# Kernel tuning notes

Measured on AMD Instinct MI355X. Metric: run time of the kernel, lower is better.

The kernel has to match this reference:

```python
import jax, jax.numpy as jnp
import numpy as np

N, T, IN, HID, ST, NL, OUT = 256, 2048, 6, 128, 64, 2, 6
LAY = IN + HID  # LMSCCell layer_size = input_size + hidden_size


def setup_inputs() -> dict:
    key = jax.random.key(0)
    ks = jax.random.split(key, 8)

    def w(k, shape, fan_in):
        return jax.random.normal(k, shape, jnp.float32) / np.sqrt(fan_in).astype(np.float32)

    return {
        "X": jax.random.normal(ks[0], (N, T, IN), jnp.float32),
        "H0": jax.random.normal(ks[1], (N, ST), jnp.float32),
        # NL gated layers (layer_size -> layer_size), stored stacked, weights as (in, out)
        "Wg1": w(ks[2], (NL, LAY, LAY), LAY), "bg1": jnp.zeros((NL, LAY), jnp.float32),
        "Wg2": w(ks[3], (NL, LAY, LAY), LAY), "bg2": jnp.zeros((NL, LAY), jnp.float32),
        # final pair: alpha (exp) and beta (tanh), layer_size -> hidden
        "Wa": w(ks[4], (LAY, HID), LAY), "ba": jnp.zeros((HID,), jnp.float32),
        "Wb": w(ks[5], (LAY, HID), LAY), "bb": jnp.zeros((HID,), jnp.float32),
        # hstate: Linear(state_size -> hidden) producing S0
        "Wh": w(ks[6], (ST, HID), ST), "bh": jnp.zeros((HID,), jnp.float32),
        # sstate2: Linear(hidden -> out_size)
        "Wo": w(ks[7], (HID, OUT), HID), "bo": jnp.zeros((OUT,), jnp.float32),
    }


def reference(X, H0, Wg1, bg1, Wg2, bg2, Wa, ba, Wb, bb, Wh, bh, Wo, bo):
    # hstate: initial hidden state for the LMSC recurrence
    S0 = H0 @ Wh + bh  # (N, HID)

    def step(H, x_t):
        # x_t: (N, IN); H: (N, HID)
        norm = jnp.linalg.norm(x_t, axis=1, keepdims=True)  # (N, 1)
        Lv = jnp.concatenate([x_t / norm, H], axis=1)       # (N, LAY)
        for i in range(NL):  # small fixed layer count, structurally distinct weights
            Lv = jnp.tanh(Lv @ Wg1[i] + bg1[i]) * jnp.tanh(Lv @ Wg2[i] + bg2[i])
        alpha = jnp.exp(Lv @ Wa + ba)   # (N, HID)
        beta = jnp.tanh(Lv @ Wb + bb)   # (N, HID)
        Hn = jnp.exp(-alpha * norm) * (H - beta) + beta
        return Hn, Hn

    _, Ys = jax.lax.scan(step, S0, jnp.swapaxes(X, 0, 1))  # (T, N, HID)
    Y = jnp.swapaxes(Ys, 0, 1)  # (N, T, HID)
    return Y @ Wo + bo          # (N, T, OUT)
```

## Files before the change

### kernel.cpp

```cpp
#include <hip/hip_runtime.h>

#define Nb   256
#define Tt   2048
#define INs  6
#define HID  128
#define STs  64
#define LAY  134
#define OUTs 6
#define NPAIR 67
#define NDW  68

typedef _Float16 h2 __attribute__((ext_vector_type(2)));
typedef __fp16  f16x2 __attribute__((ext_vector_type(2)));

__device__ __forceinline__ float exp2_fast(float x) {
#if __has_builtin(__builtin_amdgcn_exp2f)
    return __builtin_amdgcn_exp2f(x);
#else
    return exp2f(x);
#endif
}
__device__ __forceinline__ float rcp_fast(float x) {
#if __has_builtin(__builtin_amdgcn_rcpf)
    return __builtin_amdgcn_rcpf(x);
#else
    return 1.0f / x;
#endif
}
__device__ __forceinline__ float tanh_fast(float x) {
    float e = exp2_fast(x * 2.8853900817779268f);
    return 1.0f - 2.0f * rcp_fast(e + 1.0f);
}
__device__ __forceinline__ unsigned pack2(float a, float b) {
#if __has_builtin(__builtin_amdgcn_cvt_pkrtz)
    union { f16x2 h; unsigned u; } u;
    u.h = __builtin_amdgcn_cvt_pkrtz(a, b);
    return u.u;
#else
    union { h2 h; unsigned u; } u;
    u.h[0] = (_Float16)a; u.h[1] = (_Float16)b;
    return u.u;
#endif
}
__device__ __forceinline__ h2 as_h2(unsigned v) {
    union { unsigned u; h2 h; } u; u.u = v; return u.h;
}
__device__ __forceinline__ float dot2f(h2 a, h2 b, float c) {
#if __has_builtin(__builtin_amdgcn_fdot2)
    union { h2 h; f16x2 f; } ua, ub;
    ua.h = a; ub.h = b;
    return __builtin_amdgcn_fdot2(ua.f, ub.f, c, false);
#else
    return c + (float)a[0] * (float)b[0] + (float)a[1] * (float)b[1];
#endif
}

__device__ __forceinline__ float dotLv(const unsigned* buf, const h2* w, float bias) {
    const uint4* b4 = (const uint4*)buf;
    float a0 = 0.f, a1 = 0.f, a2 = 0.f, a3 = 0.f;
#pragma unroll
    for (int m = 0; m < 17; ++m) {
        uint4 v = b4[m];
        a0 = dot2f(as_h2(v.x), w[4*m+0], a0);
        a1 = dot2f(as_h2(v.y), w[4*m+1], a1);
        a2 = dot2f(as_h2(v.z), w[4*m+2], a2);
        a3 = dot2f(as_h2(v.w), w[4*m+3], a3);
    }
    return ((a0 + a1) + (a2 + a3)) + bias;
}

__device__ __forceinline__ void do_proj(const float* Hrow, const float* wo0, const float* wo1,
                                        const float* bo6, float* outp, int l) {
    float hA = Hrow[2*l], hB = Hrow[2*l+1];
    float r[6];
#pragma unroll
    for (int o = 0; o < 6; ++o) r[o] = hA * wo0[o] + hB * wo1[o];
#pragma unroll
    for (int o = 0; o < 6; ++o) {
#pragma unroll
        for (int k = 1; k < 64; k <<= 1) r[o] += __shfl_xor(r[o], k, 64);
    }
    if (l == 0) {
#pragma unroll
        for (int o = 0; o < 6; ++o) outp[o] = r[o] + bo6[o];
    }
}

__global__ __launch_bounds__(1024)
void lmsc_kernel(const float* __restrict__ X,  const float* __restrict__ H0,
                 const float* __restrict__ Wg1, const float* __restrict__ bg1,
                 const float* __restrict__ Wg2, const float* __restrict__ bg2,
                 const float* __restrict__ Wa,  const float* __restrict__ ba,
                 const float* __restrict__ Wb,  const float* __restrict__ bb,
                 const float* __restrict__ Wh,  const float* __restrict__ bh,
                 const float* __restrict__ Wo,  const float* __restrict__ bo,
                 float* __restrict__ out)
{
    __shared__ float Xls[Tt * INs];
    __shared__ alignas(16) unsigned LvX[NDW];
    __shared__ alignas(16) unsigned LvB[NDW];
    __shared__ float T1[LAY], T2[LAY];
    __shared__ float Hf[2][HID];
    __shared__ float Aal[HID], Bbe[HID];
    __shared__ float H0l[STs];
    __shared__ float nrm[2], rnr[2];

    const int tid = threadIdx.x;
    const int n   = blockIdx.x;

    {
        const float4* Xg  = (const float4*)(X + (size_t)n * (Tt * INs));
        float4*       Xl4 = (float4*)Xls;
        for (int i = tid; i < (Tt * INs) / 4; i += 1024) Xl4[i] = Xg[i];
    }
    if (tid < STs) H0l[tid] = H0[n * STs + tid];

    h2 wreg[NDW];
    float bias = 0.f;
    {
        const float* Wp = nullptr; int od = LAY, j = 0;
        if      (tid < 134) { Wp = Wg1;             j = tid;       bias = bg1[j]; }
        else if (tid < 268) { Wp = Wg2;             j = tid - 134; bias = bg2[j]; }
        else if (tid < 402) { Wp = Wg1 + LAY*LAY;   j = tid - 268; bias = bg1[LAY + j]; }
        else if (tid < 536) { Wp = Wg2 + LAY*LAY;   j = tid - 402; bias = bg2[LAY + j]; }
        else if (tid < 664) { Wp = Wa; od = HID;    j = tid - 536; bias = ba[j]; }
        else if (tid < 792) { Wp = Wb; od = HID;    j = tid - 664; bias = bb[j]; }
        if (Wp) {
            for (int m = 0; m < NPAIR; ++m) {
                float w0 = Wp[(2*m)     * od + j];
                float w1 = Wp[(2*m + 1) * od + j];
                h2 h; h[0] = (_Float16)w0; h[1] = (_Float16)w1;
                wreg[m] = h;
            }
            h2 z; z[0] = (_Float16)0.f; z[1] = (_Float16)0.f;
            wreg[NPAIR] = z;
        }
    }
    float wo0[6], wo1[6], bo6[6];
    if (tid >= 960) {
        int l = tid - 960;
#pragma unroll
        for (int o = 0; o < 6; ++o) {
            wo0[o] = Wo[(2*l)     * OUTs + o];
            wo1[o] = Wo[(2*l + 1) * OUTs + o];
            bo6[o] = bo[o];
        }
    }
    __syncthreads();

    if (tid >= 536 && tid < 664) {
        int j = tid - 536;
        float s = bh[j];
        for (int k = 0; k < STs; ++k) s += H0l[k] * Wh[k * HID + j];
        Hf[0][j] = s;
        ((_Float16*)LvX)[6 + j] = (_Float16)s;
    }
    if (tid == 900) {
        float s = 0.f;
#pragma unroll
        for (int i = 0; i < 6; ++i) s += Xls[i] * Xls[i];
        float nv = sqrtf(s);
        float rn = rcp_fast(nv);
        nrm[0] = nv; rnr[0] = rn;
        LvX[0] = pack2(Xls[0]*rn, Xls[1]*rn);
        LvX[1] = pack2(Xls[2]*rn, Xls[3]*rn);
        LvX[2] = pack2(Xls[4]*rn, Xls[5]*rn);
    }
    if (tid == 0) { LvX[NPAIR] = 0u; LvB[NPAIR] = 0u; }
    __syncthreads();

    const float LOG2E = 1.4426950408889634f;

#pragma unroll 1
    for (int t = 0; t < Tt; ++t) {
        const int p = t & 1;
        if (tid < 268) {
            float s = dotLv(LvX, wreg, bias);
            float v = tanh_fast(s);
            if (tid < 134) T1[tid] = v; else T2[tid - 134] = v;
        } else if (tid >= 960) {
            if (t > 0)
                do_proj(Hf[p], wo0, wo1, bo6, out + ((size_t)n * Tt + (t - 1)) * OUTs, tid - 960);
        } else if (tid == 900 && (t + 1) < Tt) {
            const float* xp = &Xls[(t + 1) * INs];
            float s = 0.f;
#pragma unroll
            for (int i = 0; i < 6; ++i) s += xp[i] * xp[i];
            float nv = sqrtf(s);
            nrm[(t + 1) & 1] = nv;
            rnr[(t + 1) & 1] = rcp_fast(nv);
        }
        __syncthreads();
        if (tid >= 800 && tid < 800 + NPAIR) {
            int m = tid - 800;
            float p0 = T1[2*m]     * T2[2*m];
            float p1 = T1[2*m + 1] * T2[2*m + 1];
            LvB[m] = pack2(p0, p1);
        } else if (tid == 900 && (t + 1) < Tt) {
            const float* xp = &Xls[(t + 1) * INs];
            float rn = rnr[(t + 1) & 1];
            LvX[0] = pack2(xp[0]*rn, xp[1]*rn);
            LvX[1] = pack2(xp[2]*rn, xp[3]*rn);
            LvX[2] = pack2(xp[4]*rn, xp[5]*rn);
        }
        __syncthreads();
        if (tid >= 268 && tid < 536) {
            float s = dotLv(LvB, wreg, bias);
            float v = tanh_fast(s);
            if (tid < 402) T1[tid - 268] = v; else T2[tid - 402] = v;
        }
        __syncthreads();
        if (tid >= 800 && tid < 800 + NPAIR) {
            int m = tid - 800;
            float p0 = T1[2*m]     * T2[2*m];
            float p1 = T1[2*m + 1] * T2[2*m + 1];
            LvB[m] = pack2(p0, p1);
        }
        __syncthreads();
        if (tid >= 536 && tid < 792) {
            float s = dotLv(LvB, wreg, bias);
            if (tid < 664) Aal[tid - 536] = exp2_fast(s * LOG2E);
            else           Bbe[tid - 664] = tanh_fast(s);
        }
        __syncthreads();
        if (tid < HID) {
            float a = Aal[tid], b = Bbe[tid];
            float h = Hf[p][tid];
            float e = exp2_fast(-a * nrm[p] * LOG2E);
            float hn = e * (h - b) + b;
            Hf[p ^ 1][tid] = hn;
            ((_Float16*)LvX)[6 + tid] = (_Float16)hn;
        }
        __syncthreads();
    }
    if (tid >= 960)
        do_proj(Hf[Tt & 1], wo0, wo1, bo6, out + ((size_t)n * Tt + (Tt - 1)) * OUTs, tid - 960);
}

extern "C" void kernel_launch(void* const* d_in, const int* in_sizes, int n_in,
                              void* d_out, int out_size, void* d_ws, size_t ws_size,
                              hipStream_t stream) {
    const float* X   = (const float*)d_in[0];
    const float* H0  = (const float*)d_in[1];
    const float* Wg1 = (const float*)d_in[2];
    const float* bg1 = (const float*)d_in[3];
    const float* Wg2 = (const float*)d_in[4];
    const float* bg2 = (const float*)d_in[5];
    const float* Wa  = (const float*)d_in[6];
    const float* ba  = (const float*)d_in[7];
    const float* Wb  = (const float*)d_in[8];
    const float* bb  = (const float*)d_in[9];
    const float* Wh  = (const float*)d_in[10];
    const float* bh  = (const float*)d_in[11];
    const float* Wo  = (const float*)d_in[12];
    const float* bo  = (const float*)d_in[13];
    float* out = (float*)d_out;

    hipLaunchKernelGGL(lmsc_kernel, dim3(Nb), dim3(1024), 0, stream,
                       X, H0, Wg1, bg1, Wg2, bg2, Wa, ba, Wb, bb, Wh, bh, Wo, bo, out);
}
```

Baseline: 3.902 ms.

## Fuse paired gate dot products per thread and halve block size

```diff
diff --git a/kernel.cpp b/kernel.cpp
--- a/kernel.cpp
+++ b/kernel.cpp
@@ -55,18 +55,22 @@
 #endif
 }
 
-__device__ __forceinline__ float dotLv(const unsigned* buf, const h2* w, float bias) {
+__device__ __forceinline__ void dotLv2(const unsigned* buf, const h2* w1, const h2* w2,
+                                       float b1, float b2, float& o1, float& o2) {
     const uint4* b4 = (const uint4*)buf;
     float a0 = 0.f, a1 = 0.f, a2 = 0.f, a3 = 0.f;
+    float c0 = 0.f, c1 = 0.f, c2 = 0.f, c3 = 0.f;
 #pragma unroll
     for (int m = 0; m < 17; ++m) {
         uint4 v = b4[m];
-        a0 = dot2f(as_h2(v.x), w[4*m+0], a0);
-        a1 = dot2f(as_h2(v.y), w[4*m+1], a1);
-        a2 = dot2f(as_h2(v.z), w[4*m+2], a2);
-        a3 = dot2f(as_h2(v.w), w[4*m+3], a3);
-    }
-    return ((a0 + a1) + (a2 + a3)) + bias;
+        h2 vx = as_h2(v.x), vy = as_h2(v.y), vz = as_h2(v.z), vw = as_h2(v.w);
+        a0 = dot2f(vx, w1[4*m+0], a0);  c0 = dot2f(vx, w2[4*m+0], c0);
+        a1 = dot2f(vy, w1[4*m+1], a1);  c1 = dot2f(vy, w2[4*m+1], c1);
+        a2 = dot2f(vz, w1[4*m+2], a2);  c2 = dot2f(vz, w2[4*m+2], c2);
+        a3 = dot2f(vw, w1[4*m+3], a3);  c3 = dot2f(vw, w2[4*m+3], c3);
+    }
+    o1 = ((a0 + a1) + (a2 + a3)) + b1;
+    o2 = ((c0 + c1) + (c2 + c3)) + b2;
 }
 
 __device__ __forceinline__ void do_proj(const float* Hrow, const float* wo0, const float* wo1,
@@ -86,7 +90,7 @@
     }
 }
 
-__global__ __launch_bounds__(1024)
+__global__ __launch_bounds__(512, 2)
 void lmsc_kernel(const float* __restrict__ X,  const float* __restrict__ H0,
                  const float* __restrict__ Wg1, const float* __restrict__ bg1,
                  const float* __restrict__ Wg2, const float* __restrict__ bg2,
@@ -99,9 +103,8 @@
     __shared__ float Xls[Tt * INs];
     __shared__ alignas(16) unsigned LvX[NDW];
     __shared__ alignas(16) unsigned LvB[NDW];
-    __shared__ float T1[LAY], T2[LAY];
-    __shared__ float Hf[2][HID];
-    __shared__ float Aal[HID], Bbe[HID];
+    __shared__ alignas(16) unsigned LvC[NDW];
+    __shared__ float Hf[HID];
     __shared__ float H0l[STs];
     __shared__ float nrm[2], rnr[2];
 
@@ -111,34 +114,38 @@
     {
         const float4* Xg  = (const float4*)(X + (size_t)n * (Tt * INs));
         float4*       Xl4 = (float4*)Xls;
-        for (int i = tid; i < (Tt * INs) / 4; i += 1024) Xl4[i] = Xg[i];
+        for (int i = tid; i < (Tt * INs) / 4; i += 512) Xl4[i] = Xg[i];
     }
     if (tid < STs) H0l[tid] = H0[n * STs + tid];
-
-    h2 wreg[NDW];
-    float bias = 0.f;
+    if (tid == 0) { LvX[NDW-1] = 0u; LvB[NDW-1] = 0u; LvC[NDW-1] = 0u; }
+
+    h2 w1[NDW], w2[NDW];
+    float b1 = 0.f, b2 = 0.f;
     {
-        const float* Wp = nullptr; int od = LAY, j = 0;
-        if      (tid < 134) { Wp = Wg1;             j = tid;       bias = bg1[j]; }
-        else if (tid < 268) { Wp = Wg2;             j = tid - 134; bias = bg2[j]; }
-        else if (tid < 402) { Wp = Wg1 + LAY*LAY;   j = tid - 268; bias = bg1[LAY + j]; }
-        else if (tid < 536) { Wp = Wg2 + LAY*LAY;   j = tid - 402; bias = bg2[LAY + j]; }
-        else if (tid < 664) { Wp = Wa; od = HID;    j = tid - 536; bias = ba[j]; }
-        else if (tid < 792) { Wp = Wb; od = HID;    j = tid - 664; bias = bb[j]; }
-        if (Wp) {
+        const float* Wp1 = nullptr; const float* Wp2 = nullptr; int od = LAY, j = 0;
+        if (tid < 134) {
+            Wp1 = Wg1;             Wp2 = Wg2;             j = tid;
+            b1 = bg1[j];           b2 = bg2[j];
+        } else if (tid >= 192 && tid < 326) {
+            Wp1 = Wg1 + LAY*LAY;   Wp2 = Wg2 + LAY*LAY;   j = tid - 192;
+            b1 = bg1[LAY + j];     b2 = bg2[LAY + j];
+        } else if (tid >= 384) {
+            Wp1 = Wa; Wp2 = Wb; od = HID;                 j = tid - 384;
+            b1 = ba[j];            b2 = bb[j];
+        }
+        if (Wp1) {
             for (int m = 0; m < NPAIR; ++m) {
-                float w0 = Wp[(2*m)     * od + j];
-                float w1 = Wp[(2*m + 1) * od + j];
-                h2 h; h[0] = (_Float16)w0; h[1] = (_Float16)w1;
-                wreg[m] = h;
+                h2 a; a[0] = (_Float16)Wp1[(2*m) * od + j]; a[1] = (_Float16)Wp1[(2*m+1) * od + j];
+                h2 b; b[0] = (_Float16)Wp2[(2*m) * od + j]; b[1] = (_Float16)Wp2[(2*m+1) * od + j];
+                w1[m] = a; w2[m] = b;
             }
-            h2 z; z[0] = (_Float16)0.f; z[1] = (_Float16)0.f;
-            wreg[NPAIR] = z;
-        }
+        }
+        h2 z; z[0] = (_Float16)0.f; z[1] = (_Float16)0.f;
+        w1[NPAIR] = z; w2[NPAIR] = z;
     }
     float wo0[6], wo1[6], bo6[6];
-    if (tid >= 960) {
-        int l = tid - 960;
+    if (tid >= 384 && tid < 448) {
+        int l = tid - 384;
 #pragma unroll
         for (int o = 0; o < 6; ++o) {
             wo0[o] = Wo[(2*l)     * OUTs + o];
@@ -148,14 +155,17 @@
     }
     __syncthreads();
 
-    if (tid >= 536 && tid < 664) {
-        int j = tid - 536;
+    float h = 0.f;
+    if (tid >= 384) {
+        int j = tid - 384;
         float s = bh[j];
         for (int k = 0; k < STs; ++k) s += H0l[k] * Wh[k * HID + j];
-        Hf[0][j] = s;
+        h = s;
+        Hf[j] = s;
         ((_Float16*)LvX)[6 + j] = (_Float16)s;
     }
-    if (tid == 900) {
+    if (tid == 448 - 64) {}
+    if (tid == 448) {
         float s = 0.f;
 #pragma unroll
         for (int i = 0; i < 6; ++i) s += Xls[i] * Xls[i];
@@ -166,7 +176,6 @@
         LvX[1] = pack2(Xls[2]*rn, Xls[3]*rn);
         LvX[2] = pack2(Xls[4]*rn, Xls[5]*rn);
     }
-    if (tid == 0) { LvX[NPAIR] = 0u; LvB[NPAIR] = 0u; }
     __syncthreads();
 
     const float LOG2E = 1.4426950408889634f;
@@ -174,14 +183,15 @@
 #pragma unroll 1
     for (int t = 0; t < Tt; ++t) {
         const int p = t & 1;
-        if (tid < 268) {
-            float s = dotLv(LvX, wreg, bias);
-            float v = tanh_fast(s);
-            if (tid < 134) T1[tid] = v; else T2[tid - 134] = v;
-        } else if (tid >= 960) {
+        if (tid < 134) {
+            float s1, s2;
+            dotLv2(LvX, w1, w2, b1, b2, s1, s2);
+            float v = tanh_fast(s1) * tanh_fast(s2);
+            ((_Float16*)LvB)[tid] = (_Float16)v;
+        } else if (tid >= 384 && tid < 448) {
             if (t > 0)
-                do_proj(Hf[p], wo0, wo1, bo6, out + ((size_t)n * Tt + (t - 1)) * OUTs, tid - 960);
-        } else if (tid == 900 && (t + 1) < Tt) {
+                do_proj(Hf, wo0, wo1, bo6, out + ((size_t)n * Tt + (t - 1)) * OUTs, tid - 384);
+        } else if (tid == 448 && (t + 1) < Tt) {
             const float* xp = &Xls[(t + 1) * INs];
             float s = 0.f;
 #pragma unroll
@@ -191,12 +201,12 @@
             rnr[(t + 1) & 1] = rcp_fast(nv);
         }
         __syncthreads();
-        if (tid >= 800 && tid < 800 + NPAIR) {
-            int m = tid - 800;
-            float p0 = T1[2*m]     * T2[2*m];
-            float p1 = T1[2*m + 1] * T2[2*m + 1];
-            LvB[m] = pack2(p0, p1);
-        } else if (tid == 900 && (t + 1) < Tt) {
+        if (tid >= 192 && tid < 326) {
+            float s1, s2;
+            dotLv2(LvB, w1, w2, b1, b2, s1, s2);
+            float v = tanh_fast(s1) * tanh_fast(s2);
+            ((_Float16*)LvC)[tid - 192] = (_Float16)v;
+        } else if (tid == 0 && (t + 1) < Tt) {
             const float* xp = &Xls[(t + 1) * INs];
             float rn = rnr[(t + 1) & 1];
             LvX[0] = pack2(xp[0]*rn, xp[1]*rn);
@@ -204,37 +214,21 @@
             LvX[2] = pack2(xp[4]*rn, xp[5]*rn);
         }
         __syncthreads();
-        if (tid >= 268 && tid < 536) {
-            float s = dotLv(LvB, wreg, bias);
-            float v = tanh_fast(s);
-            if (tid < 402) T1[tid - 268] = v; else T2[tid - 402] = v;
+        if (tid >= 384) {
+            int j = tid - 384;
+            float sA, sB;
+            dotLv2(LvC, w1, w2, b1, b2, sA, sB);
+            float a = exp2_fast(sA * LOG2E);
+            float b = tanh_fast(sB);
+            float e = exp2_fast(-a * nrm[p] * LOG2E);
+            h = e * (h - b) + b;
+            Hf[j] = h;
+            ((_Float16*)LvX)[6 + j] = (_Float16)h;
         }
         __syncthreads();
-        if (tid >= 800 && tid < 800 + NPAIR) {
-            int m = tid - 800;
-            float p0 = T1[2*m]     * T2[2*m];
-            float p1 = T1[2*m + 1] * T2[2*m + 1];
-            LvB[m] = pack2(p0, p1);
-        }
-        __syncthreads();
-        if (tid >= 536 && tid < 792) {
-            float s = dotLv(LvB, wreg, bias);
-            if (tid < 664) Aal[tid - 536] = exp2_fast(s * LOG2E);
-            else           Bbe[tid - 664] = tanh_fast(s);
-        }
-        __syncthreads();
-        if (tid < HID) {
-            float a = Aal[tid], b = Bbe[tid];
-            float h = Hf[p][tid];
-            float e = exp2_fast(-a * nrm[p] * LOG2E);
-            float hn = e * (h - b) + b;
-            Hf[p ^ 1][tid] = hn;
-            ((_Float16*)LvX)[6 + tid] = (_Float16)hn;
-        }
-        __syncthreads();
-    }
-    if (tid >= 960)
-        do_proj(Hf[Tt & 1], wo0, wo1, bo6, out + ((size_t)n * Tt + (Tt - 1)) * OUTs, tid - 960);
+    }
+    if (tid >= 384 && tid < 448)
+        do_proj(Hf, wo0, wo1, bo6, out + ((size_t)n * Tt + (Tt - 1)) * OUTs, tid - 384);
 }
 
 extern "C" void kernel_launch(void* const* d_in, const int* in_sizes, int n_in,
@@ -256,6 +250,6 @@
     const float* bo  = (const float*)d_in[13];
     float* out = (float*)d_out;
 
-    hipLaunchKernelGGL(lmsc_kernel, dim3(Nb), dim3(1024), 0, stream,
+    hipLaunchKernelGGL(lmsc_kernel, dim3(Nb), dim3(512), 0, stream,
                        X, H0, Wg1, bg1, Wg2, bg2, Wa, ba, Wb, bb, Wh, bh, Wo, bo, out);
 }
```

Result: faster. 3.537 ms (-9.3%).
